# Kernel optimization log

Hardware: AMD Instinct MI355X
Metric: run time of the kernel (lower is better)

The kernel has to match this reference:

```python
import jax, jax.numpy as jnp
import numpy as np

N_CHARS, EMB, HID, SEQ = 256, 512, 2048, 4096

def setup_inputs() -> dict:
    key = jax.random.key(0)
    ks = jax.random.split(key, 13)
    s = lambda k, shape: jax.random.normal(k, shape, dtype=jnp.float32) * 0.02
    return {
        "input_seq": jax.random.randint(ks[0], (SEQ,), 0, N_CHARS, dtype=jnp.int32),
        "emb_table": s(ks[1], (N_CHARS, EMB)),
        "Wf": s(ks[2], (HID, EMB + HID)), "bf": s(ks[3], (HID,)),
        "Wi": s(ks[4], (HID, EMB + HID)), "bi": s(ks[5], (HID,)),
        "Wo": s(ks[6], (HID, EMB + HID)), "bo": s(ks[7], (HID,)),
        "Wc": s(ks[8], (HID, EMB + HID)), "bc": s(ks[9], (HID,)),
        "Wy": s(ks[10], (N_CHARS, HID)), "by": s(ks[11], (N_CHARS,)),
    }

def reference(input_seq, emb_table, Wf, bf, Wi, bi, Wo, bo, Wc, bc, Wy, by):
    E = emb_table.shape[1]
    embs = emb_table[input_seq]  # [T, E]
    # Split each gate Linear on concat([emb, h]) into input and recurrent parts.
    # Input contributions for all timesteps as one GEMM per gate: [T, H]
    xf = embs @ Wf[:, :E].T + bf
    xi = embs @ Wi[:, :E].T + bi
    xo = embs @ Wo[:, :E].T + bo
    xc = embs @ Wc[:, :E].T + bc
    Wfh, Wih, Woh, Wch = Wf[:, E:], Wi[:, E:], Wo[:, E:], Wc[:, E:]

    def step(carry, xs):
        h, c = carry
        xf_t, xi_t, xo_t, xc_t = xs
        ft = jax.nn.sigmoid(xf_t + Wfh @ h)
        it = jax.nn.sigmoid(xi_t + Wih @ h)
        tct = jnp.tanh(xc_t + Wch @ h)
        c_new = ft * c + it * tct
        ot = jax.nn.sigmoid(xo_t + Woh @ h)
        h_new = ot * jnp.tanh(c_new)
        o = Wy @ h_new + by
        return (h_new, c_new), o

    h0 = jnp.zeros((Wf.shape[0],), dtype=embs.dtype)
    c0 = jnp.zeros((Wf.shape[0],), dtype=embs.dtype)
    (h, c), outs = jax.lax.scan(step, (h0, c0), (xf, xi, xo, xc))
    return outs, h, c
```

## Files before the change

### kernel.cpp

```cpp
#include <hip/hip_runtime.h>
#include <hip/hip_fp16.h>

#define SEQL 4096
#define EMBD 512
#define HIDD 2048
#define NCH  256
#define WCOL 2560

typedef _Float16 half8_t  __attribute__((ext_vector_type(8)));
typedef _Float16 half2_t  __attribute__((ext_vector_type(2)));
typedef float    float4_t __attribute__((ext_vector_type(4)));
typedef unsigned uint4_t  __attribute__((ext_vector_type(4)));
typedef unsigned uint2_t  __attribute__((ext_vector_type(2)));

#if __has_builtin(__builtin_amdgcn_fdot2)
__device__ __forceinline__ float fdot2u(unsigned a, unsigned b, float c) {
  return __builtin_amdgcn_fdot2(__builtin_bit_cast(half2_t, a),
                                __builtin_bit_cast(half2_t, b), c, false);
}
#else
__device__ __forceinline__ float fdot2u(unsigned a, unsigned b, float c) {
  half2_t ha = __builtin_bit_cast(half2_t, a), hb = __builtin_bit_cast(half2_t, b);
  return c + (float)ha.x * (float)hb.x + (float)ha.y * (float)hb.y;
}
#endif

__device__ __forceinline__ float sigm_f(float x)  { return 1.f / (1.f + __expf(-x)); }
__device__ __forceinline__ float tanh_f(float x)  { return 1.f - 2.f / (__expf(2.f * x) + 1.f); }

__device__ __forceinline__ uint4_t poll_ld(const unsigned* p) {
  uint4_t r;
  asm volatile("global_load_dwordx4 %0, %1, off sc1\n\ts_waitcnt vmcnt(0)"
               : "=v"(r) : "v"(p) : "memory");
  return r;
}

__global__ void prep_kernel(const int* __restrict__ seq, const float* __restrict__ emb,
                            const float* __restrict__ Wf, const float* __restrict__ Wi,
                            const float* __restrict__ Wo, const float* __restrict__ Wc,
                            const float* __restrict__ Wy,
                            _Float16* __restrict__ emb16, _Float16* __restrict__ Wst16,
                            _Float16* __restrict__ Wy16, unsigned* __restrict__ hx)
{
  const long nEmb = (long)SEQL * EMBD;
  const long nWst = (long)4 * HIDD * EMBD;
  const long nWy  = (long)NCH * HIDD;
  const long nHx  = 2 * HIDD;
  const long total = nEmb + nWst + nWy + nHx;
  long stride = (long)gridDim.x * blockDim.x;
  for (long i = (long)blockIdx.x * blockDim.x + threadIdx.x; i < total; i += stride) {
    if (i < nEmb) {
      long t = i >> 9, e = i & 511;
      emb16[i] = (_Float16)emb[(long)seq[t] * EMBD + e];
    } else if (i < nEmb + nWst) {
      long j = i - nEmb;
      long row = j >> 9, k = j & 511;
      long r = row >> 11, jr = row & 2047;
      const float* W = (r == 0) ? Wf : (r == 1) ? Wi : (r == 2) ? Wo : Wc;
      Wst16[j] = (_Float16)W[jr * WCOL + k];
    } else if (i < nEmb + nWst + nWy) {
      long j = i - nEmb - nWst;
      Wy16[j] = (_Float16)Wy[j];
    } else {
      hx[i - nEmb - nWst - nWy] = 0u;
    }
  }
}

template<int K, int MODE>
__global__ __launch_bounds__(256) void gemm_bt(const _Float16* __restrict__ A,
                                               const _Float16* __restrict__ B,
                                               _Float16* __restrict__ C16,
                                               float* __restrict__ Cf,
                                               const float* __restrict__ bias, int N)
{
  __shared__ _Float16 At[128 * 32];
  __shared__ _Float16 Bt[128 * 32];
  const int tid = threadIdx.x;
  const int w = tid >> 6, lane = tid & 63;
  const int wm = w >> 1, wn = w & 1;
  const int lr = lane & 15, kg = lane >> 4;
  const long tm = (long)blockIdx.y * 128;
  const long tn = (long)blockIdx.x * 128;

  float4_t acc[4][4];
#pragma unroll
  for (int a = 0; a < 4; a++)
#pragma unroll
    for (int b = 0; b < 4; b++) acc[a][b] = (float4_t)0.f;

  for (int kt = 0; kt < K; kt += 32) {
    __syncthreads();
#pragma unroll
    for (int s = 0; s < 2; s++) {
      int l = s * 256 + tid;
      int row = l >> 2, ks = (l & 3) * 8;
      *(uint4*)&At[row * 32 + ks] = *(const uint4*)&A[(tm + row) * (long)K + kt + ks];
      *(uint4*)&Bt[row * 32 + ks] = *(const uint4*)&B[(tn + row) * (long)K + kt + ks];
    }
    __syncthreads();
    half8_t af[4], bf[4];
#pragma unroll
    for (int mi = 0; mi < 4; mi++) af[mi] = *(const half8_t*)&At[(wm * 64 + mi * 16 + lr) * 32 + kg * 8];
#pragma unroll
    for (int ni = 0; ni < 4; ni++) bf[ni] = *(const half8_t*)&Bt[(wn * 64 + ni * 16 + lr) * 32 + kg * 8];
#pragma unroll
    for (int mi = 0; mi < 4; mi++)
#pragma unroll
      for (int ni = 0; ni < 4; ni++)
        acc[mi][ni] = __builtin_amdgcn_mfma_f32_16x16x32_f16(af[mi], bf[ni], acc[mi][ni], 0, 0, 0);
  }

#pragma unroll
  for (int mi = 0; mi < 4; mi++)
#pragma unroll
    for (int ni = 0; ni < 4; ni++)
#pragma unroll
      for (int i = 0; i < 4; i++) {
        long gm = tm + wm * 64 + mi * 16 + kg * 4 + i;
        long gn = tn + wn * 64 + ni * 16 + lr;
        float v = acc[mi][ni][i];
        if (MODE == 0) C16[gm * (long)N + gn] = (_Float16)v;
        else           Cf[gm * (long)N + gn] = v + bias[gn];
      }
}

__global__ __launch_bounds__(512) void lstm_seq(
    const _Float16* __restrict__ xq,
    const float* __restrict__ Wf, const float* __restrict__ Wi,
    const float* __restrict__ Wo, const float* __restrict__ Wc,
    const float* __restrict__ bfp, const float* __restrict__ bip,
    const float* __restrict__ bop, const float* __restrict__ bcp,
    unsigned* __restrict__ hx,
    _Float16* __restrict__ H16,
    float* __restrict__ out)
{
  __shared__ uint2_t hbuf2[2][512];

  const int tid  = threadIdx.x;
  const int w    = tid >> 6, lane = tid & 63;
  const int rw   = lane >> 4, hsub = lane & 15;
  const int g    = blockIdx.x;
  const int jg   = g * 8 + w;

  const float* Wsel = (rw == 0) ? Wf : (rw == 1) ? Wi : (rw == 2) ? Wo : Wc;
  const float* bsel = (rw == 0) ? bfp : (rw == 1) ? bip : (rw == 2) ? bop : bcp;
  const float* wrow = Wsel + (long)jg * WCOL + EMBD;

  uint2 wreg[32];
#pragma unroll
  for (int it = 0; it < 32; ++it) {
    const float4 wv = *(const float4*)(wrow + it * 64 + hsub * 4);
    half2_t lo = { (_Float16)wv.x, (_Float16)wv.y };
    half2_t hi = { (_Float16)wv.z, (_Float16)wv.w };
    wreg[it].x = __builtin_bit_cast(unsigned, lo);
    wreg[it].y = __builtin_bit_cast(unsigned, hi);
  }
  const float bias = (hsub == 0) ? bsel[jg] : 0.f;

  float c = 0.f;

  for (int t = 0; t < SEQL; ++t) {
    const int par = t & 1;
    float xv = 0.f;
    if (hsub == 0) xv = (float)xq[(long)t * 8192 + rw * HIDD + jg];

    if (t == 0) {
      uint2_t z; z.x = 0u; z.y = 0u;
      hbuf2[0][tid] = z;
    } else {
      const unsigned* slice = hx + (long)par * HIDD + tid * 4;
      const unsigned tg = (unsigned)t;
      uint4_t v;
      int guard = 0;
      for (;;) {
        v = poll_ld(slice);
        if (((v.x >> 16) == tg) & ((v.y >> 16) == tg) &
            ((v.z >> 16) == tg) & ((v.w >> 16) == tg)) break;
        if (++guard > (1 << 22)) break;
      }
      uint2_t p;
      p.x = (v.x & 0xffffu) | (v.y << 16);
      p.y = (v.z & 0xffffu) | (v.w << 16);
      hbuf2[par][tid] = p;
    }
    __syncthreads();

    float a0 = 0.f, a1 = 0.f, a2 = 0.f, a3 = 0.f;
#pragma unroll
    for (int it = 0; it < 32; ++it) {
      const uint2_t hv = hbuf2[par][it * 16 + hsub];
      if (it & 1) { a2 = fdot2u(wreg[it].x, hv.x, a2); a3 = fdot2u(wreg[it].y, hv.y, a3); }
      else        { a0 = fdot2u(wreg[it].x, hv.x, a0); a1 = fdot2u(wreg[it].y, hv.y, a1); }
    }
    float s = (a0 + a1) + (a2 + a3);
    s += __shfl_xor(s, 1, 64);
    s += __shfl_xor(s, 2, 64);
    s += __shfl_xor(s, 4, 64);
    s += __shfl_xor(s, 8, 64);

    float act = 0.f;
    if (hsub == 0) {
      const float pre = s + xv + bias;
      act = (rw == 3) ? tanh_f(pre) : sigm_f(pre);
    }
    const float af = __shfl(act, 0,  64);
    const float ai = __shfl(act, 16, 64);
    const float ao = __shfl(act, 32, 64);
    const float ac = __shfl(act, 48, 64);

    if (lane == 0) {
      c = af * c + ai * ac;
      const float h = ao * tanh_f(c);
      const _Float16 hh = (_Float16)h;
      const unsigned pk = (unsigned)__builtin_bit_cast(unsigned short, hh)
                        | ((unsigned)(t + 1) << 16);
      __hip_atomic_store(hx + (long)((t + 1) & 1) * HIDD + jg, pk,
                         __ATOMIC_RELAXED, __HIP_MEMORY_SCOPE_AGENT);
      H16[(long)t * HIDD + jg] = hh;
      if (t == SEQL - 1) {
        out[(long)SEQL * NCH + jg] = h;
        out[(long)SEQL * NCH + HIDD + jg] = c;
      }
    }
  }
}

extern "C" void kernel_launch(void* const* d_in, const int* in_sizes, int n_in,
                              void* d_out, int out_size, void* d_ws, size_t ws_size,
                              hipStream_t stream) {
  const int*   seq = (const int*)d_in[0];
  const float* emb = (const float*)d_in[1];
  const float* Wf  = (const float*)d_in[2];
  const float* bf_ = (const float*)d_in[3];
  const float* Wi  = (const float*)d_in[4];
  const float* bi_ = (const float*)d_in[5];
  const float* Wo  = (const float*)d_in[6];
  const float* bo_ = (const float*)d_in[7];
  const float* Wc  = (const float*)d_in[8];
  const float* bc_ = (const float*)d_in[9];
  const float* Wy  = (const float*)d_in[10];
  const float* by  = (const float*)d_in[11];
  float* out = (float*)d_out;

  char* ws = (char*)d_ws;
  _Float16* xq     = (_Float16*)(ws);
  _Float16* emb16  = (_Float16*)(ws + (64ll << 20));
  _Float16* Wst16  = (_Float16*)(ws + (68ll << 20));
  _Float16* Wy16   = (_Float16*)(ws + (76ll << 20));
  _Float16* H16    = (_Float16*)(ws + (77ll << 20));
  unsigned* hx     = (unsigned*)(ws + (93ll << 20));

  prep_kernel<<<2048, 256, 0, stream>>>(seq, emb, Wf, Wi, Wo, Wc, Wy,
                                        emb16, Wst16, Wy16, hx);

  dim3 g1(8192 / 128, 4096 / 128);
  gemm_bt<EMBD, 0><<<g1, 256, 0, stream>>>(emb16, Wst16, xq, nullptr, nullptr, 8192);

  lstm_seq<<<256, 512, 0, stream>>>(xq, Wf, Wi, Wo, Wc, bf_, bi_, bo_, bc_,
                                    hx, H16, out);

  dim3 g2(NCH / 128, 4096 / 128);
  gemm_bt<HIDD, 1><<<g2, 256, 0, stream>>>(H16, Wy16, nullptr, out, by, NCH);
}
```

Baseline: 8.391 ms.

## Relay hidden state through per-XCD local buffer to cut cross-die polling

Each XCD elects one relay block via an atomic claim. The relay polls the global hidden-state buffer and copies the slice into a per-XCD local buffer. The other blocks poll that local copy with sc0 loads and fall back to the global buffer every 32 iterations. H16 writes move from per-lane scalar stores to vectorized row writes by one block in eight, taken from shared memory one step later, with a final poll to write the last step. This aims to cut coherent cross-die polling traffic in the per-step barrier, but it adds a relay hop of latency and relies on sc0 visibility within an XCD.

After: 30.74 ms. 266% more time.

```diff
diff --git a/kernel.cpp b/kernel.cpp
--- a/kernel.cpp
+++ b/kernel.cpp
@@ -34,18 +34,29 @@
                : "=v"(r) : "v"(p) : "memory");
   return r;
 }
+__device__ __forceinline__ uint4_t poll_ld_sc0(const unsigned* p) {
+  uint4_t r;
+  asm volatile("global_load_dwordx4 %0, %1, off sc0\n\ts_waitcnt vmcnt(0)"
+               : "=v"(r) : "v"(p) : "memory");
+  return r;
+}
+__device__ __forceinline__ int ok4(uint4_t v, unsigned tg) {
+  return ((v.x >> 16) == tg) & ((v.y >> 16) == tg) &
+         ((v.z >> 16) == tg) & ((v.w >> 16) == tg);
+}
 
 __global__ void prep_kernel(const int* __restrict__ seq, const float* __restrict__ emb,
                             const float* __restrict__ Wf, const float* __restrict__ Wi,
                             const float* __restrict__ Wo, const float* __restrict__ Wc,
                             const float* __restrict__ Wy,
                             _Float16* __restrict__ emb16, _Float16* __restrict__ Wst16,
-                            _Float16* __restrict__ Wy16, unsigned* __restrict__ hx)
+                            _Float16* __restrict__ Wy16, unsigned* __restrict__ hx,
+                            int* __restrict__ claim)
 {
   const long nEmb = (long)SEQL * EMBD;
   const long nWst = (long)4 * HIDD * EMBD;
   const long nWy  = (long)NCH * HIDD;
-  const long nHx  = 2 * HIDD;
+  const long nHx  = 2 * HIDD + 8;
   const long total = nEmb + nWst + nWy + nHx;
   long stride = (long)gridDim.x * blockDim.x;
   for (long i = (long)blockIdx.x * blockDim.x + threadIdx.x; i < total; i += stride) {
@@ -62,7 +73,9 @@
       long j = i - nEmb - nWst;
       Wy16[j] = (_Float16)Wy[j];
     } else {
-      hx[i - nEmb - nWst - nWy] = 0u;
+      long j = i - nEmb - nWst - nWy;
+      if (j < 2 * HIDD) hx[j] = 0u;
+      else              claim[j - 2 * HIDD] = 0;
     }
   }
 }
@@ -132,16 +145,25 @@
     const float* __restrict__ bfp, const float* __restrict__ bip,
     const float* __restrict__ bop, const float* __restrict__ bcp,
     unsigned* __restrict__ hx,
+    unsigned* __restrict__ hxl,
+    int*      __restrict__ claim,
     _Float16* __restrict__ H16,
     float* __restrict__ out)
 {
   __shared__ uint2_t hbuf2[2][512];
+  __shared__ int meta[1];
 
   const int tid  = threadIdx.x;
   const int w    = tid >> 6, lane = tid & 63;
   const int rw   = lane >> 4, hsub = lane & 15;
   const int g    = blockIdx.x;
   const int jg   = g * 8 + w;
+  const int rowWriter = ((g & 7) == 0);
+
+  unsigned xcc;
+  asm volatile("s_getreg_b32 %0, hwreg(20, 0, 32)" : "=s"(xcc));
+  xcc &= 7;
+  if (tid == 0) meta[0] = (atomicCAS(&claim[xcc], 0, 1) == 0) ? 1 : 0;
 
   const float* Wsel = (rw == 0) ? Wf : (rw == 1) ? Wi : (rw == 2) ? Wo : Wc;
   const float* bsel = (rw == 0) ? bfp : (rw == 1) ? bip : (rw == 2) ? bop : bcp;
@@ -158,6 +180,10 @@
   }
   const float bias = (hsub == 0) ? bsel[jg] : 0.f;
 
+  __syncthreads();
+  const int isRelay = meta[0];
+  unsigned* hloc = hxl + (long)xcc * 2 * HIDD;
+
   float c = 0.f;
 
   for (int t = 0; t < SEQL; ++t) {
@@ -169,15 +195,29 @@
       uint2_t z; z.x = 0u; z.y = 0u;
       hbuf2[0][tid] = z;
     } else {
-      const unsigned* slice = hx + (long)par * HIDD + tid * 4;
+      const unsigned* gsl = hx + (long)par * HIDD + tid * 4;
       const unsigned tg = (unsigned)t;
       uint4_t v;
       int guard = 0;
-      for (;;) {
-        v = poll_ld(slice);
-        if (((v.x >> 16) == tg) & ((v.y >> 16) == tg) &
-            ((v.z >> 16) == tg) & ((v.w >> 16) == tg)) break;
-        if (++guard > (1 << 22)) break;
+      if (isRelay) {
+        for (;;) {
+          v = poll_ld(gsl);
+          if (ok4(v, tg)) break;
+          if (++guard > (1 << 22)) break;
+        }
+        *(uint4_t*)(hloc + (long)par * HIDD + tid * 4) = v;
+      } else {
+        const unsigned* lsl = hloc + (long)par * HIDD + tid * 4;
+        for (;;) {
+          v = poll_ld_sc0(lsl);
+          if (ok4(v, tg)) break;
+          ++guard;
+          if ((guard & 31) == 31) {
+            uint4_t u = poll_ld(gsl);
+            if (ok4(u, tg)) { v = u; break; }
+          }
+          if (guard > (1 << 22)) break;
+        }
       }
       uint2_t p;
       p.x = (v.x & 0xffffu) | (v.y << 16);
@@ -185,6 +225,10 @@
       hbuf2[par][tid] = p;
     }
     __syncthreads();
+
+    if (rowWriter && t > 0 && tid < 16) {
+      *(uint2_t*)&H16[(long)(t - 1) * HIDD + g * 8 + tid * 4] = hbuf2[par][g * 2 + tid];
+    }
 
     float a0 = 0.f, a1 = 0.f, a2 = 0.f, a3 = 0.f;
 #pragma unroll
@@ -217,12 +261,26 @@
                         | ((unsigned)(t + 1) << 16);
       __hip_atomic_store(hx + (long)((t + 1) & 1) * HIDD + jg, pk,
                          __ATOMIC_RELAXED, __HIP_MEMORY_SCOPE_AGENT);
-      H16[(long)t * HIDD + jg] = hh;
       if (t == SEQL - 1) {
         out[(long)SEQL * NCH + jg] = h;
         out[(long)SEQL * NCH + HIDD + jg] = c;
       }
     }
+  }
+
+  if (rowWriter && tid < 16) {
+    const unsigned* fsl = hx + (long)(SEQL & 1) * HIDD + g * 8 + tid * 4;
+    const unsigned tg = (unsigned)SEQL;
+    uint4_t v; int guard = 0;
+    for (;;) {
+      v = poll_ld(fsl);
+      if (ok4(v, tg)) break;
+      if (++guard > (1 << 22)) break;
+    }
+    uint2_t p;
+    p.x = (v.x & 0xffffu) | (v.y << 16);
+    p.y = (v.z & 0xffffu) | (v.w << 16);
+    *(uint2_t*)&H16[(long)(SEQL - 1) * HIDD + g * 8 + tid * 4] = p;
   }
 }
 
@@ -250,15 +308,17 @@
   _Float16* Wy16   = (_Float16*)(ws + (76ll << 20));
   _Float16* H16    = (_Float16*)(ws + (77ll << 20));
   unsigned* hx     = (unsigned*)(ws + (93ll << 20));
+  unsigned* hxl    = (unsigned*)(ws + (93ll << 20) + (16 << 10));
+  int*      claim  = (int*)(ws + (93ll << 20) + (144 << 10));
 
   prep_kernel<<<2048, 256, 0, stream>>>(seq, emb, Wf, Wi, Wo, Wc, Wy,
-                                        emb16, Wst16, Wy16, hx);
+                                        emb16, Wst16, Wy16, hx, claim);
 
   dim3 g1(8192 / 128, 4096 / 128);
   gemm_bt<EMBD, 0><<<g1, 256, 0, stream>>>(emb16, Wst16, xq, nullptr, nullptr, 8192);
 
   lstm_seq<<<256, 512, 0, stream>>>(xq, Wf, Wi, Wo, Wc, bf_, bi_, bo_, bc_,
-                                    hx, H16, out);
+                                    hx, hxl, claim, H16, out);
 
   dim3 g2(NCH / 128, 4096 / 128);
   gemm_bt<HIDD, 1><<<g2, 256, 0, stream>>>(H16, Wy16, nullptr, out, by, NCH);
```

## Add a helper wavefront per block for input prefetch and batched h publishing

Applied to the files above, without the earlier changes.

Each LSTM block gets a ninth wavefront. It prefetches the precomputed input projections into shared memory in blocks of 32 timesteps, gathers the eight per-wave h values through shared memory, and publishes them to global memory with the step-tag stores plus the H16 writes. The compute waves lose the global xq load and the global stores on their critical path. The polling check also becomes a wave-wide __all vote. In exchange there is an extra wave, extra LDS traffic, and another handoff stage (a shared-memory flag spin) between h being computed and h becoming visible to other blocks, which may add latency on the serial critical path.

Measured after the change: 11.80 ms. +40.6%, slower.

```diff
diff --git a/kernel.cpp b/kernel.cpp
--- a/kernel.cpp
+++ b/kernel.cpp
@@ -33,6 +33,10 @@
   asm volatile("global_load_dwordx4 %0, %1, off sc1\n\ts_waitcnt vmcnt(0)"
                : "=v"(r) : "v"(p) : "memory");
   return r;
+}
+__device__ __forceinline__ int ok4(uint4_t v, unsigned tg) {
+  return ((v.x >> 16) == tg) & ((v.y >> 16) == tg) &
+         ((v.z >> 16) == tg) & ((v.w >> 16) == tg);
 }
 
 __global__ void prep_kernel(const int* __restrict__ seq, const float* __restrict__ emb,
@@ -125,7 +129,7 @@
       }
 }
 
-__global__ __launch_bounds__(512) void lstm_seq(
+__global__ __launch_bounds__(576) void lstm_seq(
     const _Float16* __restrict__ xq,
     const float* __restrict__ Wf, const float* __restrict__ Wi,
     const float* __restrict__ Wo, const float* __restrict__ Wc,
@@ -136,91 +140,127 @@
     float* __restrict__ out)
 {
   __shared__ uint2_t hbuf2[2][512];
+  __shared__ uint4_t xbufv[2][32][4];
+  __shared__ unsigned hpub[8];
 
   const int tid  = threadIdx.x;
   const int w    = tid >> 6, lane = tid & 63;
-  const int rw   = lane >> 4, hsub = lane & 15;
   const int g    = blockIdx.x;
-  const int jg   = g * 8 + w;
-
-  const float* Wsel = (rw == 0) ? Wf : (rw == 1) ? Wi : (rw == 2) ? Wo : Wc;
-  const float* bsel = (rw == 0) ? bfp : (rw == 1) ? bip : (rw == 2) ? bop : bcp;
-  const float* wrow = Wsel + (long)jg * WCOL + EMBD;
-
-  uint2 wreg[32];
-#pragma unroll
-  for (int it = 0; it < 32; ++it) {
-    const float4 wv = *(const float4*)(wrow + it * 64 + hsub * 4);
-    half2_t lo = { (_Float16)wv.x, (_Float16)wv.y };
-    half2_t hi = { (_Float16)wv.z, (_Float16)wv.w };
-    wreg[it].x = __builtin_bit_cast(unsigned, lo);
-    wreg[it].y = __builtin_bit_cast(unsigned, hi);
-  }
-  const float bias = (hsub == 0) ? bsel[jg] : 0.f;
-
-  float c = 0.f;
-
-  for (int t = 0; t < SEQL; ++t) {
-    const int par = t & 1;
-    float xv = 0.f;
-    if (hsub == 0) xv = (float)xq[(long)t * 8192 + rw * HIDD + jg];
-
-    if (t == 0) {
-      uint2_t z; z.x = 0u; z.y = 0u;
-      hbuf2[0][tid] = z;
-    } else {
-      const unsigned* slice = hx + (long)par * HIDD + tid * 4;
-      const unsigned tg = (unsigned)t;
-      uint4_t v;
+
+  if (tid < 8) hpub[tid] = 0u;
+
+  if (w < 8) {
+    const int rw   = lane >> 4, hsub = lane & 15;
+    const int jg   = g * 8 + w;
+
+    const float* Wsel = (rw == 0) ? Wf : (rw == 1) ? Wi : (rw == 2) ? Wo : Wc;
+    const float* bsel = (rw == 0) ? bfp : (rw == 1) ? bip : (rw == 2) ? bop : bcp;
+    const float* wrow = Wsel + (long)jg * WCOL + EMBD;
+
+    uint2 wreg[32];
+#pragma unroll
+    for (int it = 0; it < 32; ++it) {
+      const float4 wv = *(const float4*)(wrow + it * 64 + hsub * 4);
+      half2_t lo = { (_Float16)wv.x, (_Float16)wv.y };
+      half2_t hi = { (_Float16)wv.z, (_Float16)wv.w };
+      wreg[it].x = __builtin_bit_cast(unsigned, lo);
+      wreg[it].y = __builtin_bit_cast(unsigned, hi);
+    }
+    const float bias = (hsub == 0) ? bsel[jg] : 0.f;
+
+    float c = 0.f;
+
+    for (int t = 0; t < SEQL; ++t) {
+      const int par = t & 1;
+      if (t == 0) {
+        uint2_t z; z.x = 0u; z.y = 0u;
+        hbuf2[0][tid] = z;
+      } else {
+        const unsigned* slice = hx + (long)par * HIDD + tid * 4;
+        const unsigned tg = (unsigned)t;
+        uint4_t v;
+        int guard = 0;
+        for (;;) {
+          v = poll_ld(slice);
+          if (__all(ok4(v, tg))) break;
+          if (++guard > (1 << 22)) break;
+        }
+        uint2_t p;
+        p.x = (v.x & 0xffffu) | (v.y << 16);
+        p.y = (v.z & 0xffffu) | (v.w << 16);
+        hbuf2[par][tid] = p;
+      }
+      __syncthreads();
+
+      float a0 = 0.f, a1 = 0.f, a2 = 0.f, a3 = 0.f;
+#pragma unroll
+      for (int it = 0; it < 32; ++it) {
+        const uint2_t hv = hbuf2[par][it * 16 + hsub];
+        if (it & 1) { a2 = fdot2u(wreg[it].x, hv.x, a2); a3 = fdot2u(wreg[it].y, hv.y, a3); }
+        else        { a0 = fdot2u(wreg[it].x, hv.x, a0); a1 = fdot2u(wreg[it].y, hv.y, a1); }
+      }
+      float s = (a0 + a1) + (a2 + a3);
+      s += __shfl_xor(s, 1, 64);
+      s += __shfl_xor(s, 2, 64);
+      s += __shfl_xor(s, 4, 64);
+      s += __shfl_xor(s, 8, 64);
+
+      float act = 0.f;
+      if (hsub == 0) {
+        const float xv = (float)((const _Float16*)&xbufv[(t >> 5) & 1][t & 31][rw])[w];
+        const float pre = s + xv + bias;
+        act = (rw == 3) ? tanh_f(pre) : sigm_f(pre);
+      }
+      const float af = __shfl(act, 0,  64);
+      const float ai = __shfl(act, 16, 64);
+      const float ao = __shfl(act, 32, 64);
+      const float ac = __shfl(act, 48, 64);
+
+      if (lane == 0) {
+        c = af * c + ai * ac;
+        const float h = ao * tanh_f(c);
+        const _Float16 hh = (_Float16)h;
+        const unsigned pk = (unsigned)__builtin_bit_cast(unsigned short, hh)
+                          | ((unsigned)(t + 1) << 16);
+        ((volatile unsigned*)hpub)[w] = pk;
+        if (t == SEQL - 1) {
+          out[(long)SEQL * NCH + jg] = h;
+          out[(long)SEQL * NCH + HIDD + jg] = c;
+        }
+      }
+    }
+  } else {
+    auto fetch_block = [&](int b) {
+#pragma unroll
+      for (int q = 0; q < 2; ++q) {
+        const int cidx = lane + (q << 6);
+        const int t_off = cidx >> 2, r = cidx & 3;
+        const uint4_t* src = (const uint4_t*)(xq + ((long)(b * 32 + t_off) << 13)
+                                                 + (r << 11) + (g << 3));
+        xbufv[b & 1][t_off][r] = *src;
+      }
+    };
+    fetch_block(0);
+
+    for (int t = 0; t < SEQL; ++t) {
+      __syncthreads();
+      const unsigned tg = (unsigned)(t + 1);
+      unsigned pk = tg << 16;
       int guard = 0;
       for (;;) {
-        v = poll_ld(slice);
-        if (((v.x >> 16) == tg) & ((v.y >> 16) == tg) &
-            ((v.z >> 16) == tg) & ((v.w >> 16) == tg)) break;
-        if (++guard > (1 << 22)) break;
-      }
-      uint2_t p;
-      p.x = (v.x & 0xffffu) | (v.y << 16);
-      p.y = (v.z & 0xffffu) | (v.w << 16);
-      hbuf2[par][tid] = p;
-    }
-    __syncthreads();
-
-    float a0 = 0.f, a1 = 0.f, a2 = 0.f, a3 = 0.f;
-#pragma unroll
-    for (int it = 0; it < 32; ++it) {
-      const uint2_t hv = hbuf2[par][it * 16 + hsub];
-      if (it & 1) { a2 = fdot2u(wreg[it].x, hv.x, a2); a3 = fdot2u(wreg[it].y, hv.y, a3); }
-      else        { a0 = fdot2u(wreg[it].x, hv.x, a0); a1 = fdot2u(wreg[it].y, hv.y, a1); }
-    }
-    float s = (a0 + a1) + (a2 + a3);
-    s += __shfl_xor(s, 1, 64);
-    s += __shfl_xor(s, 2, 64);
-    s += __shfl_xor(s, 4, 64);
-    s += __shfl_xor(s, 8, 64);
-
-    float act = 0.f;
-    if (hsub == 0) {
-      const float pre = s + xv + bias;
-      act = (rw == 3) ? tanh_f(pre) : sigm_f(pre);
-    }
-    const float af = __shfl(act, 0,  64);
-    const float ai = __shfl(act, 16, 64);
-    const float ao = __shfl(act, 32, 64);
-    const float ac = __shfl(act, 48, 64);
-
-    if (lane == 0) {
-      c = af * c + ai * ac;
-      const float h = ao * tanh_f(c);
-      const _Float16 hh = (_Float16)h;
-      const unsigned pk = (unsigned)__builtin_bit_cast(unsigned short, hh)
-                        | ((unsigned)(t + 1) << 16);
-      __hip_atomic_store(hx + (long)((t + 1) & 1) * HIDD + jg, pk,
-                         __ATOMIC_RELAXED, __HIP_MEMORY_SCOPE_AGENT);
-      H16[(long)t * HIDD + jg] = hh;
-      if (t == SEQL - 1) {
-        out[(long)SEQL * NCH + jg] = h;
-        out[(long)SEQL * NCH + HIDD + jg] = c;
+        if (lane < 8) pk = ((volatile unsigned*)hpub)[lane];
+        if (__all((pk >> 16) == tg)) break;
+        if (++guard > (1 << 24)) break;
+      }
+      if (lane < 8) {
+        __hip_atomic_store(hx + (long)((t + 1) & 1) * HIDD + g * 8 + lane, pk,
+                           __ATOMIC_RELAXED, __HIP_MEMORY_SCOPE_AGENT);
+        const unsigned short lo = (unsigned short)(pk & 0xffffu);
+        H16[(long)t * HIDD + g * 8 + lane] = __builtin_bit_cast(_Float16, lo);
+      }
+      if ((t & 31) == 0) {
+        const int nb = (t >> 5) + 1;
+        if (nb < SEQL / 32) fetch_block(nb);
       }
     }
   }
@@ -257,7 +297,7 @@
   dim3 g1(8192 / 128, 4096 / 128);
   gemm_bt<EMBD, 0><<<g1, 256, 0, stream>>>(emb16, Wst16, xq, nullptr, nullptr, 8192);
 
-  lstm_seq<<<256, 512, 0, stream>>>(xq, Wf, Wi, Wo, Wc, bf_, bi_, bo_, bc_,
+  lstm_seq<<<256, 576, 0, stream>>>(xq, Wf, Wi, Wo, Wc, bf_, bi_, bo_, bc_,
                                     hx, H16, out);
 
   dim3 g2(NCH / 128, 4096 / 128);
```
